# Optimization experiments

Measured on AMD Instinct MI355X. Metric: run time of the kernel, lower is better.

Reference implementation:

```python
import jax, jax.numpy as jnp
import numpy as np

SR = 44100
LOWEST = 82.0
L_ORDER = 5
NUM_COEFF = L_ORDER + 1          # 6
NUM_ACTIVE = NUM_COEFF + 1       # 7 (linear interp)
K = int(SR // LOWEST) + NUM_ACTIVE  # coeff_vector_size = 544
N_FRAMES = 100
EXC_FRAMES = 100
EXC_ORDER = 5
BURST_LEN = 2048
N_SAMPLES = 44100


def upsample_linear(frames, T):
    """Linear interpolation of (F,) or (F, C) control frames to T samples (align_corners)."""
    F_ = frames.shape[0]
    pos = jnp.linspace(0.0, F_ - 1.0, T)
    i0 = jnp.clip(jnp.floor(pos).astype(jnp.int32), 0, F_ - 2)
    w = pos - i0.astype(pos.dtype)
    lo = frames[i0]
    hi = frames[i0 + 1]
    if frames.ndim == 2:
        w = w[:, None]
    return lo + (hi - lo) * w


def sample_wise_lpc(x, A):
    """Time-varying all-pole filter: y[t] = x[t] - sum_k A[t,k] * y[t-k-1].
    x: (T,), A: (T, N) -> y: (T,)"""
    N = A.shape[1]

    def step(buf, inp):
        xt, at = inp
        y = xt - jnp.dot(at, buf)  # buf[0]=y[t-1], ..., buf[N-1]=y[t-N]
        buf = jnp.concatenate([y[None], buf[:-1]])
        return buf, y

    _, y = jax.lax.scan(step, jnp.zeros((N,), x.dtype), (x, A))
    return y


def _forward(delay_len_frames, excitation, raw_coeff_frames, raw_gain, exc_coefficients, n_samples):
    T = n_samples
    # --- upsample control signals to audio rate ---
    delay = upsample_linear(delay_len_frames, T)                     # (T,)
    gain = jax.nn.sigmoid(raw_gain) * 0.1 + 0.9
    sb = jax.nn.sigmoid(raw_coeff_frames)                            # (F, 6)
    coeff_frames = sb / sb.sum(axis=-1, keepdims=True) * gain        # normalized, stable
    b = upsample_linear(coeff_frames, T)                             # (T, 6)

    # --- build sparse banded A (linear fractional-delay interpolation) ---
    z_l = jnp.floor(delay).astype(jnp.int32)                         # integer delay
    alfa = delay - z_l.astype(delay.dtype)                           # fractional part
    v0 = -(1.0 - alfa) * b[:, 0]                                     # (T,)
    vmid = -(alfa[:, None] * b[:, :-1] + (1.0 - alfa)[:, None] * b[:, 1:])  # (T, 5)
    vlast = -alfa * b[:, -1]                                         # (T,)
    vals = jnp.concatenate([v0[:, None], vmid, vlast[:, None]], axis=1)     # (T, 7)
    idxs = z_l[:, None] + jnp.arange(NUM_ACTIVE)[None, :]            # (T, 7)
    A = jnp.zeros((T, K), delay.dtype).at[jnp.arange(T)[:, None], idxs].set(vals)

    # --- excitation shaping filter (requires_grad branch) ---
    burst = excitation                                               # (BURST_LEN,)
    a_exc = upsample_linear(exc_coefficients, burst.shape[0])        # (BURST_LEN, 5)
    filtered_burst = sample_wise_lpc(burst, a_exc)

    # --- Karplus-Strong loop: time-varying all-pole with banded A ---
    x = jnp.zeros((T,), burst.dtype).at[: burst.shape[0]].set(filtered_burst)
    y = sample_wise_lpc(x, A)
    return y.astype(jnp.float32)


def setup_inputs() -> dict:
    key = jax.random.key(0)
    k0, k1, k2, k3 = jax.random.split(key, 4)
    # delay in [100, 520] samples so floor(delay)+NUM_ACTIVE-1 < K = 544
    delay_len_frames = 100.0 + 420.0 * jax.random.uniform(k0, (N_FRAMES,), dtype=jnp.float32)
    excitation = jax.random.normal(k1, (BURST_LEN,), dtype=jnp.float32)
    raw_coeff_frames = jax.random.uniform(k2, (N_FRAMES, NUM_COEFF), dtype=jnp.float32,
                                          minval=-2.0, maxval=0.0)
    raw_gain = jnp.asarray(0.0, dtype=jnp.float32)
    exc_coefficients = 0.01 * jax.random.normal(k3, (EXC_FRAMES, EXC_ORDER), dtype=jnp.float32)
    return {
        "delay_len_frames": delay_len_frames,
        "excitation": excitation,
        "raw_coeff_frames": raw_coeff_frames,
        "raw_gain": raw_gain,
        "exc_coefficients": exc_coefficients,
        "n_samples": N_SAMPLES,
    }


def reference(delay_len_frames, excitation, raw_coeff_frames, raw_gain, exc_coefficients, n_samples):
    return _forward(delay_len_frames, excitation, raw_coeff_frames, raw_gain,
                    exc_coefficients, n_samples)
```

## Files before the change

kernel.cpp:

```cpp
#include <hip/hip_runtime.h>
#include <math.h>


#define T_SAMPLES 44100
#define NFRAMES   100
#define NCOEF     6
#define BURST     2048
#define EXC_ORD   5

#define HISTSZ    2120
#define GRPF      9600
#define CFBUF     9856
#define POOLF     32448

#define WS_COEF_FLOATS (T_SAMPLES * 12)
#define WS_EXC_OFF     WS_COEF_FLOATS
#define WS_EXC_FLOATS  (EXC_ORD * BURST)
#define WS_TOTAL_BYTES ((size_t)(WS_COEF_FLOATS + WS_EXC_FLOATS) * 4)

__global__ __launch_bounds__(256) void diffks_precompute(
    const float* __restrict__ delay_frames,
    const float* __restrict__ raw_coeff,
    const float* __restrict__ raw_gain,
    const float* __restrict__ exc_coeff,
    float* __restrict__ ws)
{
    int g = blockIdx.x * 256 + threadIdx.x;
    const float gain = 0.1f / (1.0f + expf(-raw_gain[0])) + 0.9f;

    if (g < T_SAMPLES) {
        const float stepT = 99.0f / (float)(T_SAMPLES - 1);
        float pos = (float)g * stepT;
        int i0 = (int)pos; if (i0 > NFRAMES - 2) i0 = NFRAMES - 2;
        float w = pos - (float)i0;

        float d0 = delay_frames[i0], d1 = delay_frames[i0 + 1];
        float delay = d0 + (d1 - d0) * w;
        int z = (int)delay;
        float alfa = delay - (float)z;

        float b[NCOEF];
        {
            float c0v[NCOEF], c1v[NCOEF];
            float s0 = 0.f, s1 = 0.f;
            #pragma unroll
            for (int j = 0; j < NCOEF; ++j) {
                c0v[j] = 1.0f / (1.0f + expf(-raw_coeff[i0 * NCOEF + j]));
                c1v[j] = 1.0f / (1.0f + expf(-raw_coeff[(i0 + 1) * NCOEF + j]));
                s0 += c0v[j]; s1 += c1v[j];
            }
            float g0 = gain / s0, g1 = gain / s1;
            #pragma unroll
            for (int j = 0; j < NCOEF; ++j) {
                float x0 = c0v[j] * g0, x1 = c1v[j] * g1;
                b[j] = x0 + (x1 - x0) * w;
            }
        }
        float oma = 1.0f - alfa;
        float v0 = -oma * b[0];
        float v1 = -(alfa * b[0] + oma * b[1]);
        float v2 = -(alfa * b[1] + oma * b[2]);
        float v3 = -(alfa * b[2] + oma * b[3]);
        float v4 = -(alfa * b[3] + oma * b[4]);
        float v5 = -(alfa * b[4] + oma * b[5]);
        float v6 = -alfa * b[5];
        float pv0 = -v0, pv1 = -v1, pv2 = -v2, pv3 = -v3;
        float pv4 = -v4, pv5 = -v5, pv6 = -v6;

        int base = g - z - 1;
        int q = base - 6;
        int off = q & 1;
        unsigned b2 = ((unsigned)q) & 2046u;

        float m0, m1, m2, m3, m4, m5, m6, m7;
        if (off) { m0 = 0.f; m1 = pv6; m2 = pv5; m3 = pv4;
                   m4 = pv3; m5 = pv2; m6 = pv1; m7 = pv0; }
        else     { m0 = pv6; m1 = pv5; m2 = pv4; m3 = pv3;
                   m4 = pv2; m5 = pv1; m6 = pv0; m7 = 0.f; }

        float4* o = (float4*)(ws + (size_t)g * 12);
        o[0] = make_float4(m0, m1, m2, m3);
        o[1] = make_float4(m4, m5, m6, m7);
        o[2] = make_float4(__int_as_float((int)b2), 0.f, 0.f, 0.f);
    } else if (g < T_SAMPLES + BURST) {
        int te = g - T_SAMPLES;
        const float stepE = 99.0f / (float)(BURST - 1);
        float pos = (float)te * stepE;
        int i0 = (int)pos; if (i0 > NFRAMES - 2) i0 = NFRAMES - 2;
        float w = pos - (float)i0;
        float* o = ws + WS_EXC_OFF + te * EXC_ORD;
        #pragma unroll
        for (int k = 0; k < EXC_ORD; ++k) {
            float a0 = exc_coeff[i0 * EXC_ORD + k];
            float a1 = exc_coeff[(i0 + 1) * EXC_ORD + k];
            o[k] = a0 + (a1 - a0) * w;
        }
    }
}

__device__ __forceinline__ void gload_lds16(const float* g, float* l) {
    __builtin_amdgcn_global_load_lds(
        (const __attribute__((address_space(1))) unsigned int*)(g),
        (__attribute__((address_space(3))) unsigned int*)(l),
        16, 0, 0);
}

__global__ __launch_bounds__(256, 1) void diffks_serial(
    const float* __restrict__ excitation,
    const float* __restrict__ ws,
    float* __restrict__ out)
{
    __shared__ float s_pool[POOLF];
    __shared__ float s_x[64][33];
    __shared__ float s_hist[HISTSZ];

    float (* const s_a)[161]   = (float(*)[161])(s_pool + 19712);
    float (* const s_tail)[32] = (float(*)[32])(s_pool + 30016);
    float (* const s_bound)[6] = (float(*)[6])(s_pool + 32064);

    const int tid  = threadIdx.x;
    const int lane = tid & 63;
    const int wv   = tid >> 6;

    for (int t = tid; t < BURST; t += 256)
        s_x[t >> 5][t & 31] = excitation[t];
    for (int i = 0; i < 8; ++i) {
        int t = tid + i * 256;
        const float* g = ws + WS_EXC_OFF + t * EXC_ORD;
        float* dst = &s_a[t >> 5][(t & 31) * 5];
        dst[0] = g[0]; dst[1] = g[1]; dst[2] = g[2];
        dst[3] = g[3]; dst[4] = g[4];
    }
    for (int i = tid; i < HISTSZ; i += 256) s_hist[i] = 0.0f;
    __syncthreads();

    if (tid < 64) {
        float st[6][5];
        #pragma unroll
        for (int r = 0; r < 6; ++r)
            #pragma unroll
            for (int k = 0; k < 5; ++k) st[r][k] = 0.0f;
        #pragma unroll
        for (int r = 1; r <= 5; ++r) st[r][r - 1] = 1.0f;

        const float* ar = &s_a[lane][0];
        const float* xr = &s_x[lane][0];
        #pragma unroll 8
        for (int i = 0; i < 32; ++i) {
            float a0 = ar[i * 5 + 0], a1 = ar[i * 5 + 1], a2 = ar[i * 5 + 2];
            float a3 = ar[i * 5 + 3], a4 = ar[i * 5 + 4];
            float xv = xr[i];
            #pragma unroll
            for (int r = 0; r < 6; ++r) {
                float acc = (r == 0) ? xv : 0.0f;
                acc = fmaf(-a0, st[r][0], acc);
                acc = fmaf(-a1, st[r][1], acc);
                acc = fmaf(-a2, st[r][2], acc);
                acc = fmaf(-a3, st[r][3], acc);
                acc = fmaf(-a4, st[r][4], acc);
                st[r][4] = st[r][3]; st[r][3] = st[r][2];
                st[r][2] = st[r][1]; st[r][1] = st[r][0];
                st[r][0] = acc;
            }
        }
        #pragma unroll
        for (int r = 0; r < 6; ++r)
            #pragma unroll
            for (int k = 0; k < 5; ++k)
                s_tail[lane][r * 5 + k] = st[r][k];
    }
    __syncthreads();

    if (tid == 0) {
        float Y[5] = {0.f, 0.f, 0.f, 0.f, 0.f};
        for (int l = 0; l < 64; ++l) {
            #pragma unroll
            for (int c = 0; c < 5; ++c) s_bound[l][c] = Y[c];
            float tl[30];
            #pragma unroll
            for (int j = 0; j < 30; ++j) tl[j] = s_tail[l][j];
            float ny[5];
            #pragma unroll
            for (int k = 0; k < 5; ++k) {
                float acc = tl[k];
                #pragma unroll
                for (int c = 1; c <= 5; ++c)
                    acc = fmaf(tl[c * 5 + k], Y[c - 1], acc);
                ny[k] = acc;
            }
            #pragma unroll
            for (int k = 0; k < 5; ++k) Y[k] = ny[k];
        }
    }
    __syncthreads();

    if (tid < 64) {
        float b0 = s_bound[lane][0], b1 = s_bound[lane][1], b2 = s_bound[lane][2];
        float b3 = s_bound[lane][3], b4 = s_bound[lane][4];
        const float* ar = &s_a[lane][0];
        float* xr = &s_x[lane][0];
        #pragma unroll 8
        for (int i = 0; i < 32; ++i) {
            float a0 = ar[i * 5 + 0], a1 = ar[i * 5 + 1], a2 = ar[i * 5 + 2];
            float a3 = ar[i * 5 + 3], a4 = ar[i * 5 + 4];
            float acc = xr[i];
            acc = fmaf(-a0, b0, acc);
            acc = fmaf(-a1, b1, acc);
            acc = fmaf(-a2, b2, acc);
            acc = fmaf(-a3, b3, acc);
            acc = fmaf(-a4, b4, acc);
            b4 = b3; b3 = b2; b2 = b1; b1 = b0; b0 = acc;
            xr[i] = acc;
        }
    }
    __syncthreads();

    const bool lane_act = (lane < 50);
    const unsigned dumpA = 2048u + (unsigned)lane;

    #define STAGE_GRP(gg)                                                      \
    {                                                                          \
        float* dstb = s_pool + ((unsigned)(gg) % 3u) * CFBUF;                  \
        const float* srcb = ws + (size_t)(gg) * GRPF + lane * 4;               \
        const int nis = ((gg) >= 55) ? 5 : 38;                                 \
        for (int i = 0; i < nis; ++i)                                          \
            gload_lds16(srcb + i * 256, dstb + i * 256);                       \
    }

    #define DECLSET(J)                                                         \
        float4 p##J##a0, p##J##a1, p##J##b0, p##J##b1;                         \
        unsigned u##J##A0, u##J##A1, u##J##A2, u##J##A3;                       \
        unsigned u##J##B0, u##J##B1, u##J##B2, u##J##B3;                       \
        unsigned w##J##A, w##J##B;                                             \
        float x##J##A, x##J##B;
    DECLSET(0) DECLSET(1) DECLSET(2) DECLSET(3)
    DECLSET(4) DECLSET(5) DECLSET(6) DECLSET(7)
    #undef DECLSET

    #define PREPJ(J, BB, WXF)                                                  \
    {                                                                          \
        int b_ = (BB); if (b_ > 440) b_ = 440;                                 \
        const float* bu_ = s_pool + ((unsigned)(b_ >> 3) % 3u) * CFBUF;        \
        const int ln_ = (b_ & 7) * 100 + lane;                                 \
        const float4* qA_ = (const float4*)(bu_ + ln_ * 12);                   \
        const float4* qB_ = (const float4*)(bu_ + (ln_ + 50) * 12);            \
        p##J##a0 = qA_[0]; p##J##a1 = qA_[1];                                  \
        const unsigned bA_ = (unsigned)__float_as_int(qA_[2].x);               \
        p##J##b0 = qB_[0]; p##J##b1 = qB_[1];                                  \
        const unsigned bB_ = (unsigned)__float_as_int(qB_[2].x);               \
        u##J##A0 = bA_;               u##J##B0 = bB_;                          \
        u##J##A1 = (bA_ + 2) & 2047u; u##J##B1 = (bB_ + 2) & 2047u;            \
        u##J##A2 = (bA_ + 4) & 2047u; u##J##B2 = (bB_ + 4) & 2047u;            \
        u##J##A3 = (bA_ + 6) & 2047u; u##J##B3 = (bB_ + 6) & 2047u;            \
        const int tA_ = b_ * 100 + lane;                                       \
        const int tB_ = tA_ + 50;                                              \
        if (WXF) {                                                             \
            x##J##A = (lane_act && tA_ < BURST)                                \
                          ? s_x[(tA_ >> 5) & 63][tA_ & 31] : 0.0f;             \
            x##J##B = (lane_act && tB_ < BURST)                                \
                          ? s_x[(tB_ >> 5) & 63][tB_ & 31] : 0.0f;             \
        } else { x##J##A = 0.0f; x##J##B = 0.0f; }                             \
        w##J##A = lane_act ? (((unsigned)tA_) & 2047u) : dumpA;                \
        w##J##B = lane_act ? (((unsigned)tB_) & 2047u) : dumpA;                \
    }

    #define PREPALL(SS, WXF)                                                   \
    {                                                                          \
        const int nb_ = (SS) * 8;                                              \
        PREPJ(0, nb_ + 0, WXF) PREPJ(1, nb_ + 1, WXF)                          \
        PREPJ(2, nb_ + 2, WXF) PREPJ(3, nb_ + 3, WXF)                          \
        PREPJ(4, nb_ + 4, WXF) PREPJ(5, nb_ + 5, WXF)                          \
        PREPJ(6, nb_ + 6, WXF) PREPJ(7, nb_ + 7, WXF)                          \
    }

    #define CBODY(J)                                                           \
    {                                                                          \
        const float2 a01_ = *(const float2*)(s_hist + u##J##A0);               \
        const float2 a23_ = *(const float2*)(s_hist + u##J##A1);               \
        const float2 a45_ = *(const float2*)(s_hist + u##J##A2);               \
        const float2 a67_ = *(const float2*)(s_hist + u##J##A3);               \
        const float2 b01_ = *(const float2*)(s_hist + u##J##B0);               \
        const float2 b23_ = *(const float2*)(s_hist + u##J##B1);               \
        const float2 b45_ = *(const float2*)(s_hist + u##J##B2);               \
        const float2 b67_ = *(const float2*)(s_hist + u##J##B3);               \
        float accA = x##J##A, accB = x##J##B;                                  \
        accA = fmaf(p##J##a1.w, a67_.y, accA);                                 \
        accB = fmaf(p##J##b1.w, b67_.y, accB);                                 \
        accA = fmaf(p##J##a1.z, a67_.x, accA);                                 \
        accB = fmaf(p##J##b1.z, b67_.x, accB);                                 \
        accA = fmaf(p##J##a1.y, a45_.y, accA);                                 \
        accB = fmaf(p##J##b1.y, b45_.y, accB);                                 \
        accA = fmaf(p##J##a1.x, a45_.x, accA);                                 \
        accB = fmaf(p##J##b1.x, b45_.x, accB);                                 \
        accA = fmaf(p##J##a0.w, a23_.y, accA);                                 \
        accB = fmaf(p##J##b0.w, b23_.y, accB);                                 \
        accA = fmaf(p##J##a0.z, a23_.x, accA);                                 \
        accB = fmaf(p##J##b0.z, b23_.x, accB);                                 \
        accA = fmaf(p##J##a0.y, a01_.y, accA);                                 \
        accB = fmaf(p##J##b0.y, b01_.y, accB);                                 \
        accA = fmaf(p##J##a0.x, a01_.x, accA);                                 \
        accB = fmaf(p##J##b0.x, b01_.x, accB);                                 \
        s_hist[w##J##A] = accA;                                                \
        s_hist[w##J##B] = accB;                                                \
    }

    #define STEPBODY(WXF)                                                      \
    {                                                                          \
        if (wv == (ss & 3)) {                                                  \
            CBODY(0) CBODY(1) CBODY(2) CBODY(3)                                \
            CBODY(4) CBODY(5) CBODY(6) CBODY(7)                                \
        }                                                                      \
        if ((ss <= 53) && (wv == ((ss + 2) & 3))) { STAGE_GRP(ss + 2) }        \
        if ((ss >= 1) && (wv == ((ss + 3) & 3))) {                             \
            const int t0_ = (ss - 1) * 800;                                    \
            _Pragma("unroll")                                                  \
            for (int i_ = 0; i_ < 12; ++i_) {                                  \
                int t_ = t0_ + i_ * 64 + lane;                                 \
                out[t_] = s_hist[((unsigned)t_) & 2047u];                      \
            }                                                                  \
            { int t_ = t0_ + 768 + lane;                                       \
              if (lane < 32) out[t_] = s_hist[((unsigned)t_) & 2047u]; }       \
        }                                                                      \
        if (wv == ((ss + 1) & 3)) {                                            \
            asm volatile("s_waitcnt vmcnt(0)" ::: "memory");                   \
            PREPALL(ss + 1, WXF)                                               \
        }                                                                      \
        asm volatile("s_waitcnt lgkmcnt(0)\n\ts_barrier" ::: "memory");        \
    }

    if (wv == 0) {
        STAGE_GRP(0)
        asm volatile("s_waitcnt vmcnt(0)" ::: "memory");
    }
    if (wv == 1) { STAGE_GRP(1) }
    __syncthreads();
    if (wv == 0) { PREPALL(0, true) }
    __syncthreads();

    #pragma unroll 1
    for (int ss = 0; ss < 2; ++ss) STEPBODY(true)
    #pragma unroll 1
    for (int ss = 2; ss < 55; ++ss) STEPBODY(false)

    if (wv == 3) { CBODY(0) }
    asm volatile("s_waitcnt lgkmcnt(0)\n\ts_barrier" ::: "memory");
    for (int t_ = 43200 + tid; t_ < T_SAMPLES; t_ += 256)
        out[t_] = s_hist[((unsigned)t_) & 2047u];

    #undef STEPBODY
    #undef CBODY
    #undef PREPALL
    #undef PREPJ
    #undef STAGE_GRP
}

#define CHUNK_FB  101
#define NCH_FB    ((T_SAMPLES + CHUNK_FB - 1) / CHUNK_FB)
#define HIST_FB   1024

__global__ __launch_bounds__(128) void diffks_fallback(
    const float* __restrict__ delay_frames,
    const float* __restrict__ excitation,
    const float* __restrict__ raw_coeff,
    const float* __restrict__ raw_gain,
    const float* __restrict__ exc_coeff,
    float* __restrict__ out)
{
    __shared__ float s_a[EXC_ORD][BURST];
    __shared__ float s_x[BURST];
    __shared__ float s_hist[HIST_FB];
    __shared__ __align__(16) float s_coef[NFRAMES][8];
    __shared__ float s_delay[NFRAMES];

    const int tid = threadIdx.x;
    const float gain = 0.1f / (1.0f + expf(-raw_gain[0])) + 0.9f;

    for (int i = tid; i < NFRAMES; i += 128) s_delay[i] = delay_frames[i];
    for (int f = tid; f < NFRAMES; f += 128) {
        float sb[NCOEF]; float s = 0.0f;
        #pragma unroll
        for (int j = 0; j < NCOEF; ++j) {
            sb[j] = 1.0f / (1.0f + expf(-raw_coeff[f * NCOEF + j]));
            s += sb[j];
        }
        float inv = gain / s;
        #pragma unroll
        for (int j = 0; j < NCOEF; ++j) s_coef[f][j] = sb[j] * inv;
        s_coef[f][6] = 0.0f; s_coef[f][7] = 0.0f;
    }
    const float stepE = 99.0f / 2047.0f;
    for (int t = tid; t < BURST; t += 128) {
        float pos = (float)t * stepE;
        int i0 = (int)pos; if (i0 > NFRAMES - 2) i0 = NFRAMES - 2;
        float w = pos - (float)i0;
        const float* c0 = exc_coeff + i0 * EXC_ORD;
        #pragma unroll
        for (int k = 0; k < EXC_ORD; ++k) {
            float a0 = c0[k], a1 = c0[k + EXC_ORD];
            s_a[k][t] = a0 + (a1 - a0) * w;
        }
        s_x[t] = excitation[t];
    }
    for (int i = tid; i < HIST_FB; i += 128) s_hist[i] = 0.0f;
    __syncthreads();

    if (tid == 0) {
        float y1 = 0.f, y2 = 0.f, y3 = 0.f, y4 = 0.f, y5 = 0.f;
        #pragma unroll 4
        for (int t = 0; t < BURST; ++t) {
            float p = s_x[t];
            p = fmaf(-s_a[1][t], y2, p);
            p = fmaf(-s_a[2][t], y3, p);
            p = fmaf(-s_a[3][t], y4, p);
            p = fmaf(-s_a[4][t], y5, p);
            float y = fmaf(-s_a[0][t], y1, p);
            s_x[t] = y;
            y5 = y4; y4 = y3; y3 = y2; y2 = y1; y1 = y;
        }
    }
    __syncthreads();

    const float stepT = 99.0f / (float)(T_SAMPLES - 1);
    for (int c = 0; c < NCH_FB; ++c) {
        int t = c * CHUNK_FB + tid;
        if (tid < CHUNK_FB && t < T_SAMPLES) {
            float pos = (float)t * stepT;
            int i0 = (int)pos; if (i0 > NFRAMES - 2) i0 = NFRAMES - 2;
            float w = pos - (float)i0;
            float d0 = s_delay[i0], d1 = s_delay[i0 + 1];
            float delay = d0 + (d1 - d0) * w;
            int z = (int)delay;
            float alfa = delay - (float)z;
            const float4* f0 = reinterpret_cast<const float4*>(s_coef[i0]);
            const float4* f1 = reinterpret_cast<const float4*>(s_coef[i0 + 1]);
            float4 c0a = f0[0], c0b = f0[1];
            float4 c1a = f1[0], c1b = f1[1];
            float b[NCOEF];
            b[0] = c0a.x + (c1a.x - c0a.x) * w;
            b[1] = c0a.y + (c1a.y - c0a.y) * w;
            b[2] = c0a.z + (c1a.z - c0a.z) * w;
            b[3] = c0a.w + (c1a.w - c0a.w) * w;
            b[4] = c0b.x + (c1b.x - c0b.x) * w;
            b[5] = c0b.y + (c1b.y - c0b.y) * w;
            float oma = 1.0f - alfa;
            float v[7];
            v[0] = -oma * b[0];
            #pragma unroll
            for (int j = 1; j <= 5; ++j) v[j] = -(alfa * b[j - 1] + oma * b[j]);
            v[6] = -alfa * b[5];
            float x = (t < BURST) ? s_x[t] : 0.0f;
            int base = t - z - 1;
            float sum = 0.0f;
            #pragma unroll
            for (int j = 0; j < 7; ++j) {
                int idx = base - j;
                float yv = s_hist[idx & (HIST_FB - 1)];
                if (idx < 0) yv = 0.0f;
                sum = fmaf(v[j], yv, sum);
            }
            float y = x - sum;
            s_hist[t & (HIST_FB - 1)] = y;
            out[t] = y;
        }
        __syncthreads();
    }
}

extern "C" void kernel_launch(void* const* d_in, const int* in_sizes, int n_in,
                              void* d_out, int out_size, void* d_ws, size_t ws_size,
                              hipStream_t stream) {
    const float* delay_frames = (const float*)d_in[0];
    const float* excitation   = (const float*)d_in[1];
    const float* raw_coeff    = (const float*)d_in[2];
    const float* raw_gain     = (const float*)d_in[3];
    const float* exc_coeff    = (const float*)d_in[4];
    float* out = (float*)d_out;

    if (ws_size >= WS_TOTAL_BYTES) {
        float* ws = (float*)d_ws;
        int gridA = (T_SAMPLES + BURST + 255) / 256;
        diffks_precompute<<<gridA, 256, 0, stream>>>(delay_frames, raw_coeff,
                                                     raw_gain, exc_coeff, ws);
        diffks_serial<<<1, 256, 0, stream>>>(excitation, ws, out);
    } else {
        diffks_fallback<<<1, 128, 0, stream>>>(delay_frames, excitation,
                                               raw_coeff, raw_gain, exc_coeff, out);
    }
}
```

Before: 147.1 us.

## Fuse pairs of serial sample-block steps when delay allows independent computation

Per pair of 100-sample blocks, the kernel checks whether the minimum delay over that span is at least 200 samples. If so, the two blocks' recurrence steps have no dependency on each other, and their LDS history loads and FMAs are interleaved in a single fused body (CB2) to shorten the serial critical path. The serial 5x5 boundary-state combine also moves from one thread to five lanes using shuffles, and the LDS loads are reordered so the longest-delay taps are issued first. This adds per-step branches and a data-dependent code path. Speed now depends on the delay values, though the result stays correct for any input.

Measured after the change: 149.1 us. About the same (+1.4%).

```diff
diff --git a/kernel.cpp b/kernel.cpp
--- a/kernel.cpp
+++ b/kernel.cpp
@@ -106,6 +106,7 @@
 }
 
 __global__ __launch_bounds__(256, 1) void diffks_serial(
+    const float* __restrict__ delay_frames,
     const float* __restrict__ excitation,
     const float* __restrict__ ws,
     float* __restrict__ out)
@@ -113,6 +114,8 @@
     __shared__ float s_pool[POOLF];
     __shared__ float s_x[64][33];
     __shared__ float s_hist[HISTSZ];
+    __shared__ int s_bfl[220];
+    __shared__ unsigned s_fuse[56];
 
     float (* const s_a)[161]   = (float(*)[161])(s_pool + 19712);
     float (* const s_tail)[32] = (float(*)[32])(s_pool + 30016);
@@ -132,6 +135,16 @@
         dst[3] = g[3]; dst[4] = g[4];
     }
     for (int i = tid; i < HISTSZ; i += 256) s_hist[i] = 0.0f;
+    if (tid < 220) {
+        const int b = 2 * tid + 1;
+        const float stf = 99.0f / 44099.0f;
+        int f0 = (int)((float)(b * 100) * stf);
+        int f1 = (int)((float)(b * 100 + 99) * stf) + 1;
+        if (f1 > 99) f1 = 99;
+        float dm = delay_frames[f0];
+        for (int f = f0 + 1; f <= f1; ++f) dm = fminf(dm, delay_frames[f]);
+        s_bfl[tid] = (dm >= 200.0f) ? 1 : 0;
+    }
     __syncthreads();
 
     if (tid < 64) {
@@ -168,28 +181,34 @@
             #pragma unroll
             for (int k = 0; k < 5; ++k)
                 s_tail[lane][r * 5 + k] = st[r][k];
-    }
-    __syncthreads();
-
-    if (tid == 0) {
-        float Y[5] = {0.f, 0.f, 0.f, 0.f, 0.f};
+    } else if (tid < 120) {
+        int p = tid - 64;
+        if (p < 55)
+            s_fuse[p] = (unsigned)(s_bfl[4 * p] | (s_bfl[4 * p + 1] << 1) |
+                                   (s_bfl[4 * p + 2] << 2) |
+                                   (s_bfl[4 * p + 3] << 3));
+        else
+            s_fuse[p] = 0u;
+    }
+    __syncthreads();
+
+    if (tid < 5) {
+        float Yk = 0.0f;
         for (int l = 0; l < 64; ++l) {
-            #pragma unroll
-            for (int c = 0; c < 5; ++c) s_bound[l][c] = Y[c];
-            float tl[30];
-            #pragma unroll
-            for (int j = 0; j < 30; ++j) tl[j] = s_tail[l][j];
-            float ny[5];
-            #pragma unroll
-            for (int k = 0; k < 5; ++k) {
-                float acc = tl[k];
-                #pragma unroll
-                for (int c = 1; c <= 5; ++c)
-                    acc = fmaf(tl[c * 5 + k], Y[c - 1], acc);
-                ny[k] = acc;
-            }
-            #pragma unroll
-            for (int k = 0; k < 5; ++k) Y[k] = ny[k];
+            s_bound[l][tid] = Yk;
+            float y0 = __shfl(Yk, 0);
+            float y1 = __shfl(Yk, 1);
+            float y2 = __shfl(Yk, 2);
+            float y3 = __shfl(Yk, 3);
+            float y4 = __shfl(Yk, 4);
+            const float* tl = &s_tail[l][0];
+            float acc = tl[tid];
+            acc = fmaf(tl[5 + tid],  y0, acc);
+            acc = fmaf(tl[10 + tid], y1, acc);
+            acc = fmaf(tl[15 + tid], y2, acc);
+            acc = fmaf(tl[20 + tid], y3, acc);
+            acc = fmaf(tl[25 + tid], y4, acc);
+            Yk = acc;
         }
     }
     __syncthreads();
@@ -227,6 +246,7 @@
             gload_lds16(srcb + i * 256, dstb + i * 256);                       \
     }
 
+    unsigned fun = 0;
     #define DECLSET(J)                                                         \
         float4 p##J##a0, p##J##a1, p##J##b0, p##J##b1;                         \
         unsigned u##J##A0, u##J##A1, u##J##A2, u##J##A3;                       \
@@ -271,18 +291,19 @@
         PREPJ(2, nb_ + 2, WXF) PREPJ(3, nb_ + 3, WXF)                          \
         PREPJ(4, nb_ + 4, WXF) PREPJ(5, nb_ + 5, WXF)                          \
         PREPJ(6, nb_ + 6, WXF) PREPJ(7, nb_ + 7, WXF)                          \
+        fun = s_fuse[SS];                                                      \
     }
 
     #define CBODY(J)                                                           \
     {                                                                          \
+        const float2 a67_ = *(const float2*)(s_hist + u##J##A3);               \
+        const float2 b67_ = *(const float2*)(s_hist + u##J##B3);               \
+        const float2 a45_ = *(const float2*)(s_hist + u##J##A2);               \
+        const float2 b45_ = *(const float2*)(s_hist + u##J##B2);               \
+        const float2 a23_ = *(const float2*)(s_hist + u##J##A1);               \
+        const float2 b23_ = *(const float2*)(s_hist + u##J##B1);               \
         const float2 a01_ = *(const float2*)(s_hist + u##J##A0);               \
-        const float2 a23_ = *(const float2*)(s_hist + u##J##A1);               \
-        const float2 a45_ = *(const float2*)(s_hist + u##J##A2);               \
-        const float2 a67_ = *(const float2*)(s_hist + u##J##A3);               \
         const float2 b01_ = *(const float2*)(s_hist + u##J##B0);               \
-        const float2 b23_ = *(const float2*)(s_hist + u##J##B1);               \
-        const float2 b45_ = *(const float2*)(s_hist + u##J##B2);               \
-        const float2 b67_ = *(const float2*)(s_hist + u##J##B3);               \
         float accA = x##J##A, accB = x##J##B;                                  \
         accA = fmaf(p##J##a1.w, a67_.y, accA);                                 \
         accB = fmaf(p##J##b1.w, b67_.y, accB);                                 \
@@ -304,11 +325,52 @@
         s_hist[w##J##B] = accB;                                                \
     }
 
+    #define CB2(J, K)                                                          \
+    {                                                                          \
+        const float2 Ja67 = *(const float2*)(s_hist + u##J##A3);               \
+        const float2 Jb67 = *(const float2*)(s_hist + u##J##B3);               \
+        const float2 Ka67 = *(const float2*)(s_hist + u##K##A3);               \
+        const float2 Kb67 = *(const float2*)(s_hist + u##K##B3);               \
+        const float2 Ja45 = *(const float2*)(s_hist + u##J##A2);               \
+        const float2 Jb45 = *(const float2*)(s_hist + u##J##B2);               \
+        const float2 Ka45 = *(const float2*)(s_hist + u##K##A2);               \
+        const float2 Kb45 = *(const float2*)(s_hist + u##K##B2);               \
+        const float2 Ja23 = *(const float2*)(s_hist + u##J##A1);               \
+        const float2 Jb23 = *(const float2*)(s_hist + u##J##B1);               \
+        const float2 Ka23 = *(const float2*)(s_hist + u##K##A1);               \
+        const float2 Kb23 = *(const float2*)(s_hist + u##K##B1);               \
+        const float2 Ja01 = *(const float2*)(s_hist + u##J##A0);               \
+        const float2 Jb01 = *(const float2*)(s_hist + u##J##B0);               \
+        const float2 Ka01 = *(const float2*)(s_hist + u##K##A0);               \
+        const float2 Kb01 = *(const float2*)(s_hist + u##K##B0);               \
+        float aJ = x##J##A, bJ = x##J##B, aK = x##K##A, bK = x##K##B;          \
+        aJ = fmaf(p##J##a1.w, Ja67.y, aJ); bJ = fmaf(p##J##b1.w, Jb67.y, bJ);  \
+        aK = fmaf(p##K##a1.w, Ka67.y, aK); bK = fmaf(p##K##b1.w, Kb67.y, bK);  \
+        aJ = fmaf(p##J##a1.z, Ja67.x, aJ); bJ = fmaf(p##J##b1.z, Jb67.x, bJ);  \
+        aK = fmaf(p##K##a1.z, Ka67.x, aK); bK = fmaf(p##K##b1.z, Kb67.x, bK);  \
+        aJ = fmaf(p##J##a1.y, Ja45.y, aJ); bJ = fmaf(p##J##b1.y, Jb45.y, bJ);  \
+        aK = fmaf(p##K##a1.y, Ka45.y, aK); bK = fmaf(p##K##b1.y, Kb45.y, bK);  \
+        aJ = fmaf(p##J##a1.x, Ja45.x, aJ); bJ = fmaf(p##J##b1.x, Jb45.x, bJ);  \
+        aK = fmaf(p##K##a1.x, Ka45.x, aK); bK = fmaf(p##K##b1.x, Kb45.x, bK);  \
+        aJ = fmaf(p##J##a0.w, Ja23.y, aJ); bJ = fmaf(p##J##b0.w, Jb23.y, bJ);  \
+        aK = fmaf(p##K##a0.w, Ka23.y, aK); bK = fmaf(p##K##b0.w, Kb23.y, bK);  \
+        aJ = fmaf(p##J##a0.z, Ja23.x, aJ); bJ = fmaf(p##J##b0.z, Jb23.x, bJ);  \
+        aK = fmaf(p##K##a0.z, Ka23.x, aK); bK = fmaf(p##K##b0.z, Kb23.x, bK);  \
+        aJ = fmaf(p##J##a0.y, Ja01.y, aJ); bJ = fmaf(p##J##b0.y, Jb01.y, bJ);  \
+        aK = fmaf(p##K##a0.y, Ka01.y, aK); bK = fmaf(p##K##b0.y, Kb01.y, bK);  \
+        aJ = fmaf(p##J##a0.x, Ja01.x, aJ); bJ = fmaf(p##J##b0.x, Jb01.x, bJ);  \
+        aK = fmaf(p##K##a0.x, Ka01.x, aK); bK = fmaf(p##K##b0.x, Kb01.x, bK);  \
+        s_hist[w##J##A] = aJ;  s_hist[w##J##B] = bJ;                           \
+        s_hist[w##K##A] = aK;  s_hist[w##K##B] = bK;                           \
+    }
+
     #define STEPBODY(WXF)                                                      \
     {                                                                          \
         if (wv == (ss & 3)) {                                                  \
-            CBODY(0) CBODY(1) CBODY(2) CBODY(3)                                \
-            CBODY(4) CBODY(5) CBODY(6) CBODY(7)                                \
+            if (fun & 1u) { CB2(0, 1) } else { CBODY(0) CBODY(1) }             \
+            if (fun & 2u) { CB2(2, 3) } else { CBODY(2) CBODY(3) }             \
+            if (fun & 4u) { CB2(4, 5) } else { CBODY(4) CBODY(5) }             \
+            if (fun & 8u) { CB2(6, 7) } else { CBODY(6) CBODY(7) }             \
         }                                                                      \
         if ((ss <= 53) && (wv == ((ss + 2) & 3))) { STAGE_GRP(ss + 2) }        \
         if ((ss >= 1) && (wv == ((ss + 3) & 3))) {                             \
@@ -348,6 +410,7 @@
         out[t_] = s_hist[((unsigned)t_) & 2047u];
 
     #undef STEPBODY
+    #undef CB2
     #undef CBODY
     #undef PREPALL
     #undef PREPJ
@@ -481,7 +544,7 @@
         int gridA = (T_SAMPLES + BURST + 255) / 256;
         diffks_precompute<<<gridA, 256, 0, stream>>>(delay_frames, raw_coeff,
                                                      raw_gain, exc_coeff, ws);
-        diffks_serial<<<1, 256, 0, stream>>>(excitation, ws, out);
+        diffks_serial<<<1, 256, 0, stream>>>(delay_frames, excitation, ws, out);
     } else {
         diffks_fallback<<<1, 128, 0, stream>>>(delay_frames, excitation,
                                                raw_coeff, raw_gain, exc_coeff, out);
```
